# Kernel tuning notes

Measured on AMD Instinct MI355X. Metric: run time of the kernel, lower is better.

## Reference

```python
import jax, jax.numpy as jnp
import numpy as np

IN_DIM = 256
DIM_MSA = 32
PAIR_DIM = 64
B, L = 1, 1024


def setup_inputs() -> dict:
    key = jax.random.key(0)
    ks = jax.random.split(key, 6)
    seq_rep = jax.random.normal(ks[0], (B, L, IN_DIM), dtype=jnp.float32)
    pair_rep = jax.random.normal(ks[1], (B, L, L, PAIR_DIM), dtype=jnp.float32)
    # nn.Linear params: W [out, in], b [out]
    W1 = jax.random.normal(ks[2], (DIM_MSA, IN_DIM), dtype=jnp.float32) * (1.0 / np.sqrt(IN_DIM))
    b1 = jax.random.normal(ks[3], (DIM_MSA,), dtype=jnp.float32) * 0.01
    W2 = jax.random.normal(ks[4], (PAIR_DIM, DIM_MSA * DIM_MSA), dtype=jnp.float32) * (1.0 / np.sqrt(DIM_MSA * DIM_MSA))
    b2 = jax.random.normal(ks[5], (PAIR_DIM,), dtype=jnp.float32) * 0.01
    return {"seq_rep": seq_rep, "pair_rep": pair_rep, "W1": W1, "b1": b1, "W2": W2, "b2": b2}


def reference(seq_rep, pair_rep, W1, b1, W2, b2):
    # proj_down1: [B,L,in_dim] -> [B,L,c] where c = dim_msa
    s = seq_rep @ W1.T + b1  # [B,L,c]
    # Original: outer[b,i,j,c,d] = s[b,i,d] * s[b,j,c]; flatten (c d); proj_down2.
    # Reassociated (same math, no B*L*L*c*d intermediate):
    # out[b,i,j,p] = sum_{c,d} W2[p, c*DIM_MSA + d] * s[b,j,c] * s[b,i,d]
    Wp = W2.reshape(PAIR_DIM, DIM_MSA, DIM_MSA)  # [p, c, d]
    tmp = jnp.einsum('bjc,pcd->bjpd', s, Wp)      # [B,L,p,d]
    out = jnp.einsum('bid,bjpd->bijp', s, tmp) + b2  # [B,L,L,p]
    out = out + pair_rep
    return out
```

## Files before the change

### kernel.cpp

```cpp
#include <hip/hip_runtime.h>
#include <hip/hip_bf16.h>

#define L_SEQ    1024
#define IN_DIM   256
#define DIM_MSA  32
#define PAIR_DIM 64

typedef float f4 __attribute__((ext_vector_type(4)));
typedef short s8 __attribute__((ext_vector_type(8)));

__device__ __forceinline__ unsigned short f2bf(float f) {
    unsigned u = __float_as_uint(f);
    u = (u + 0x7FFFu + ((u >> 16) & 1u)) >> 16;
    return (unsigned short)u;
}

__global__ void k_proj1(const float* __restrict__ seq, const float* __restrict__ W1,
                        const float* __restrict__ b1, float* __restrict__ s,
                        unsigned short* __restrict__ s_bf) {
    int t = blockIdx.x * blockDim.x + threadIdx.x;
    int i = t >> 5, c = t & 31;
    const float4* sq = (const float4*)(seq + i * IN_DIM);
    const float4* w  = (const float4*)(W1  + c * IN_DIM);
    float a0 = 0.f, a1 = 0.f, a2 = 0.f, a3 = 0.f;
#pragma unroll
    for (int d4 = 0; d4 < IN_DIM / 4; ++d4) {
        float4 x = sq[d4], y = w[d4];
        a0 += x.x * y.x;  a1 += x.y * y.y;
        a2 += x.z * y.z;  a3 += x.w * y.w;
    }
    float v = b1[c] + ((a0 + a1) + (a2 + a3));
    s[t]    = v;
    s_bf[t] = f2bf(v);
}

__global__ void k_proj2(const float* __restrict__ s, const float* __restrict__ W2,
                        unsigned short* __restrict__ tmp_bf) {
    int t = blockIdx.x * blockDim.x + threadIdx.x;
    int q = t & 7, p = (t >> 3) & 63, j = t >> 9;
    const float4* w  = (const float4*)W2;
    const float*  sj = s + j * DIM_MSA;
    float4 acc = {0.f, 0.f, 0.f, 0.f};
#pragma unroll
    for (int c = 0; c < DIM_MSA; ++c) {
        float  sc = sj[c];
        float4 wv = w[p * 256 + c * 8 + q];
        acc.x += sc * wv.x;  acc.y += sc * wv.y;
        acc.z += sc * wv.z;  acc.w += sc * wv.w;
    }
    ushort4 o;
    o.x = f2bf(acc.x);  o.y = f2bf(acc.y);
    o.z = f2bf(acc.z);  o.w = f2bf(acc.w);
    ((ushort4*)tmp_bf)[t] = o;
}

__global__ __launch_bounds__(256) void k_outer_mfma2(
    const unsigned short* __restrict__ s_bf, const unsigned short* __restrict__ tmp_bf,
    const float* __restrict__ pair, const float* __restrict__ b2,
    float* __restrict__ out) {
    __shared__ float lds[4 * 16 * 256];
    int tid = threadIdx.x;
    int w = tid >> 6, l = tid & 63;
    int n = l & 15, kg = l >> 4;
    int jb = blockIdx.x & 63;
    int it = blockIdx.x >> 6;

    s8 a = *(const s8*)(s_bf + (size_t)(it * 16 + n) * DIM_MSA + kg * 8);

    int jp0 = jb * 1024 + w * 256;
    const unsigned short* bp = tmp_bf + (size_t)(jp0 + n) * DIM_MSA + kg * 8;
    float* myl = lds + w * 4096;

#pragma unroll
    for (int t = 0; t < 16; ++t) {
        s8 b = *(const s8*)(bp + (size_t)t * 16 * DIM_MSA);
        f4 z = {0.f, 0.f, 0.f, 0.f};
        f4 c = __builtin_amdgcn_mfma_f32_16x16x32_bf16(a, b, z, 0, 0, 0);
        float* dst = myl + (kg * 4) * 256 + t * 16 + n;
        dst[0]   = c.x;
        dst[256] = c.y;
        dst[512] = c.z;
        dst[768] = c.w;
    }

    f4 b4 = *(const f4*)(b2 + ((l * 4) & 63));
    size_t rowbase = (size_t)(it * 16) * 65536 + (size_t)jp0 + l * 4;
    const float* pp = pair + rowbase;
    float*       op = out  + rowbase;

#pragma unroll 8
    for (int i = 0; i < 16; ++i) {
        f4 cc = *(const f4*)(myl + i * 256 + l * 4);
        f4 pv = *(const f4*)(pp + (size_t)i * 65536);
        f4 o  = cc + b4 + pv;
        __builtin_nontemporal_store(o, (f4*)(op + (size_t)i * 65536));
    }
}

extern "C" void kernel_launch(void* const* d_in, const int* in_sizes, int n_in,
                              void* d_out, int out_size, void* d_ws, size_t ws_size,
                              hipStream_t stream) {
    const float* seq  = (const float*)d_in[0];
    const float* pair = (const float*)d_in[1];
    const float* W1   = (const float*)d_in[2];
    const float* b1   = (const float*)d_in[3];
    const float* W2   = (const float*)d_in[4];
    const float* b2   = (const float*)d_in[5];
    float* out = (float*)d_out;

    float*          s_ws = (float*)d_ws;
    unsigned short* sbf  = (unsigned short*)(s_ws + 32768);
    unsigned short* tbf  = sbf + 32768;

    k_proj1<<<(L_SEQ * DIM_MSA) / 256, 256, 0, stream>>>(seq, W1, b1, s_ws, sbf);
    k_proj2<<<(L_SEQ * PAIR_DIM * (DIM_MSA / 4)) / 256, 256, 0, stream>>>(s_ws, W2, tbf);
    k_outer_mfma2<<<64 * 64, 256, 0, stream>>>(sbf, tbf, pair, b2, out);
}
```

Measured before the change: 112.2 us.

## Halve LDS staging per wave with two passes and XOR-swizzled layout

The outer-product kernel now processes each wave's 256 output columns in two 128-column passes. This halves the shared-memory tile from 64KB to 32KB per block, which should let more blocks reside per CU and hide more memory latency. The LDS writes use an XOR swizzle on the column group to reduce bank conflicts. The epilogue switches from float4 to float2 loads and stores of pair/out, which means more memory instructions and possibly less efficient global accesses.

Result: slower. 121.5 us (+8.3%).

```diff
diff --git a/kernel.cpp b/kernel.cpp
--- a/kernel.cpp
+++ b/kernel.cpp
@@ -7,6 +7,7 @@
 #define PAIR_DIM 64
 
 typedef float f4 __attribute__((ext_vector_type(4)));
+typedef float f2 __attribute__((ext_vector_type(2)));
 typedef short s8 __attribute__((ext_vector_type(8)));
 
 __device__ __forceinline__ unsigned short f2bf(float f) {
@@ -54,11 +55,11 @@
     ((ushort4*)tmp_bf)[t] = o;
 }
 
-__global__ __launch_bounds__(256) void k_outer_mfma2(
+__global__ __launch_bounds__(256) void k_outer_mfma3(
     const unsigned short* __restrict__ s_bf, const unsigned short* __restrict__ tmp_bf,
     const float* __restrict__ pair, const float* __restrict__ b2,
     float* __restrict__ out) {
-    __shared__ float lds[4 * 16 * 256];
+    __shared__ float lds[4 * 16 * 128];
     int tid = threadIdx.x;
     int w = tid >> 6, l = tid & 63;
     int n = l & 15, kg = l >> 4;
@@ -68,32 +69,37 @@
     s8 a = *(const s8*)(s_bf + (size_t)(it * 16 + n) * DIM_MSA + kg * 8);
 
     int jp0 = jb * 1024 + w * 256;
-    const unsigned short* bp = tmp_bf + (size_t)(jp0 + n) * DIM_MSA + kg * 8;
-    float* myl = lds + w * 4096;
+    float* slab = lds + w * 2048;
+
+    f2 bias = *(const f2*)(b2 + ((2 * l) & 63));
+    size_t rowbase = (size_t)(it * 16) * 65536 + (size_t)jp0 + 2 * l;
 
 #pragma unroll
-    for (int t = 0; t < 16; ++t) {
-        s8 b = *(const s8*)(bp + (size_t)t * 16 * DIM_MSA);
-        f4 z = {0.f, 0.f, 0.f, 0.f};
-        f4 c = __builtin_amdgcn_mfma_f32_16x16x32_bf16(a, b, z, 0, 0, 0);
-        float* dst = myl + (kg * 4) * 256 + t * 16 + n;
-        dst[0]   = c.x;
-        dst[256] = c.y;
-        dst[512] = c.z;
-        dst[768] = c.w;
-    }
+    for (int P = 0; P < 2; ++P) {
+        const unsigned short* bp =
+            tmp_bf + (size_t)(jp0 + P * 128 + n) * DIM_MSA + kg * 8;
+#pragma unroll
+        for (int t = 0; t < 8; ++t) {
+            s8 b = *(const s8*)(bp + (size_t)t * 16 * DIM_MSA);
+            f4 z = {0.f, 0.f, 0.f, 0.f};
+            f4 c = __builtin_amdgcn_mfma_f32_16x16x32_bf16(a, b, z, 0, 0, 0);
+            float* dst = slab + (kg * 4) * 128 + ((t ^ kg) * 16) + n;
+            dst[0]   = c.x;
+            dst[128] = c.y;
+            dst[256] = c.z;
+            dst[384] = c.w;
+        }
 
-    f4 b4 = *(const f4*)(b2 + ((l * 4) & 63));
-    size_t rowbase = (size_t)(it * 16) * 65536 + (size_t)jp0 + l * 4;
-    const float* pp = pair + rowbase;
-    float*       op = out  + rowbase;
-
+        const float* pp = pair + rowbase + P * 128;
+        float*       op = out  + rowbase + P * 128;
 #pragma unroll 8
-    for (int i = 0; i < 16; ++i) {
-        f4 cc = *(const f4*)(myl + i * 256 + l * 4);
-        f4 pv = *(const f4*)(pp + (size_t)i * 65536);
-        f4 o  = cc + b4 + pv;
-        __builtin_nontemporal_store(o, (f4*)(op + (size_t)i * 65536));
+        for (int i = 0; i < 16; ++i) {
+            int colphys = (2 * l) ^ (((i >> 2) & 3) << 4);
+            f2 cc = *(const f2*)(slab + i * 128 + colphys);
+            f2 pv = *(const f2*)(pp + (size_t)i * 65536);
+            f2 o  = cc + bias + pv;
+            __builtin_nontemporal_store(o, (f2*)(op + (size_t)i * 65536));
+        }
     }
 }
 
@@ -114,5 +120,5 @@
 
     k_proj1<<<(L_SEQ * DIM_MSA) / 256, 256, 0, stream>>>(seq, W1, b1, s_ws, sbf);
     k_proj2<<<(L_SEQ * PAIR_DIM * (DIM_MSA / 4)) / 256, 256, 0, stream>>>(s_ws, W2, tbf);
-    k_outer_mfma2<<<64 * 64, 256, 0, stream>>>(sbf, tbf, pair, b2, out);
+    k_outer_mfma3<<<64 * 64, 256, 0, stream>>>(sbf, tbf, pair, b2, out);
 }
```
